# Kernel tuning notes

Measured on AMD Instinct MI355X. Metric: run time of the kernel, lower is better.

Reference implementation:

```python
import jax, jax.numpy as jnp
import numpy as np

B, C, FRAMES, E, W = 8, 2, 3999, 512, 16
STEP = W // 2  # frame_step = W//2 = 8


def setup_inputs() -> dict:
    key = jax.random.key(0)
    k1, k2 = jax.random.split(key)
    dec_input = jax.random.normal(k1, (B, C, FRAMES, E), dtype=jnp.float32)
    weight = jax.random.normal(k2, (W, E), dtype=jnp.float32) * (1.0 / np.sqrt(E))
    return {"dec_input": dec_input, "weight": weight}


def overlap_and_add(signal, frame_step):
    # signal: [..., frames, frame_length] -> [..., (frames-1)*step + frame_length]
    frames, frame_length = signal.shape[-2], signal.shape[-1]
    output_size = frame_step * (frames - 1) + frame_length
    # target sample index of every element of `signal`
    idx = (jnp.arange(frames)[:, None] * frame_step
           + jnp.arange(frame_length)[None, :]).reshape(-1)  # [frames*frame_length]
    flat = signal.reshape(*signal.shape[:-2], frames * frame_length)
    out = jnp.zeros((*signal.shape[:-2], output_size), dtype=signal.dtype)
    # scatter-accumulate overlapping frames along the last axis
    return out.at[..., idx].add(flat)


def reference(dec_input, weight):
    # dec_input: [B, C, frames, E]; weight: [W, E] (nn.Linear(E, W, bias=False))
    est_source = jnp.einsum('bcle,we->bclw', dec_input, weight)  # [B, C, frames, W]
    return overlap_and_add(est_source, STEP)  # [B, C, T]
```

## Files before the change

kernel.cpp:

```cpp
#include <hip/hip_runtime.h>
#include <cstdint>
#include <cstddef>


#define NBC     16
#define FRAMES  3999
#define EE      512
#define TOUT    32000
#define NGROUP  4000
#define GPB     63
#define KCH     64
#define NKCH    8
#define XSTR    65


__global__ __launch_bounds__(256) void decoder_kernel(
    const float* __restrict__ dec,
    const float* __restrict__ wgt,
    float* __restrict__ out)
{
    __shared__ float wl[16 * EE];
    __shared__ float xs[64 * XSTR];

    const int tid   = threadIdx.x;
    const int bc    = blockIdx.x >> 6;
    const int chunk = blockIdx.x & 63;
    const int g0    = chunk * GPB;

    const float* decb = dec + (size_t)bc * (FRAMES * EE);

    {
        const float4* ws = (const float4*)wgt;
        float4*       wd = (float4*)wl;
        #pragma unroll
        for (int i = 0; i < 8; ++i)
            wd[tid + 256 * i] = ws[tid + 256 * i];
    }

    const int s = tid & 63;
    const int q = tid >> 6;
    const int f = g0 - 1 + s;
    const float vmask = (f >= 0 && f < FRAMES) ? 1.0f : 0.0f;

    const int rs = tid >> 4;
    const int c4 = tid & 15;

    float acc[16];
    #pragma unroll
    for (int w = 0; w < 16; ++w) acc[w] = 0.f;

    for (int kk = 0; kk < NKCH; ++kk) {
        __syncthreads();

        #pragma unroll
        for (int it = 0; it < 4; ++it) {
            const int r = rs + 16 * it;
            int fr = g0 - 1 + r;
            fr = min(max(fr, 0), FRAMES - 1);
            const float4 v =
                *(const float4*)(decb + (size_t)fr * EE + kk * KCH + 4 * c4);
            float* x = &xs[r * XSTR + 4 * c4];
            x[0] = v.x; x[1] = v.y; x[2] = v.z; x[3] = v.w;
        }
        __syncthreads();

        float xv[16];
        #pragma unroll
        for (int u = 0; u < 16; ++u)
            xv[u] = xs[s * XSTR + 16 * q + u];
        #pragma unroll
        for (int w = 0; w < 16; ++w) {
            const float4* wrow =
                (const float4*)&wl[w * EE + kk * KCH + 16 * q];
            float sum = 0.f;
            #pragma unroll
            for (int u = 0; u < 4; ++u) {
                const float4 wq = wrow[u];
                sum += xv[4*u+0]*wq.x + xv[4*u+1]*wq.y
                     + xv[4*u+2]*wq.z + xv[4*u+3]*wq.w;
            }
            acc[w] += sum;
        }
    }

    __syncthreads();
    float* red = xs;
    #pragma unroll
    for (int w = 0; w < 16; ++w)
        red[(q * 16 + w) * 64 + s] = acc[w] * vmask;
    __syncthreads();

    for (int o = tid; o < GPB * 8; o += 256) {
        const int j = o >> 3;
        const int i = o & 7;
        const int g = g0 + j;
        if (g < NGROUP) {
            float v = 0.f;
            #pragma unroll
            for (int qq = 0; qq < 4; ++qq)
                v += red[(qq * 16 + i) * 64 + (j + 1)]
                   + red[(qq * 16 + 8 + i) * 64 + j];
            out[(size_t)bc * TOUT + g * 8 + i] = v;
        }
    }
}

extern "C" void kernel_launch(void* const* d_in, const int* in_sizes, int n_in,
                              void* d_out, int out_size, void* d_ws, size_t ws_size,
                              hipStream_t stream) {
    const float* dec = (const float*)d_in[0];
    const float* wgt = (const float*)d_in[1];
    float* out = (float*)d_out;

    decoder_kernel<<<dim3(1024), dim3(256), 0, stream>>>(dec, wgt, out);
}
```

Baseline: 221.2 us.

## Load decoder rows directly into registers, dropping shared-memory staging of inputs

```diff
diff --git a/kernel.cpp b/kernel.cpp
--- a/kernel.cpp
+++ b/kernel.cpp
@@ -9,25 +9,20 @@
 #define TOUT    32000
 #define NGROUP  4000
 #define GPB     63
-#define KCH     64
-#define NKCH    8
-#define XSTR    65
 
-
-__global__ __launch_bounds__(256) void decoder_kernel(
+__global__ __launch_bounds__(256, 4) void decoder_kernel(
     const float* __restrict__ dec,
     const float* __restrict__ wgt,
     float* __restrict__ out)
 {
-    __shared__ float wl[16 * EE];
-    __shared__ float xs[64 * XSTR];
+    __shared__ float smem[16 * EE];
+    float* wl  = smem;
+    float* red = smem;
 
     const int tid   = threadIdx.x;
     const int bc    = blockIdx.x >> 6;
     const int chunk = blockIdx.x & 63;
     const int g0    = chunk * GPB;
-
-    const float* decb = dec + (size_t)bc * (FRAMES * EE);
 
     {
         const float4* ws = (const float4*)wgt;
@@ -36,55 +31,43 @@
         for (int i = 0; i < 8; ++i)
             wd[tid + 256 * i] = ws[tid + 256 * i];
     }
+    __syncthreads();
 
     const int s = tid & 63;
     const int q = tid >> 6;
     const int f = g0 - 1 + s;
     const float vmask = (f >= 0 && f < FRAMES) ? 1.0f : 0.0f;
+    const int fr = min(max(f, 0), FRAMES - 1);
 
-    const int rs = tid >> 4;
-    const int c4 = tid & 15;
+    const float* arow = dec + ((size_t)bc * FRAMES + fr) * EE + q * 128;
+    const float* wbase = wl + q * 128;
 
     float acc[16];
     #pragma unroll
     for (int w = 0; w < 16; ++w) acc[w] = 0.f;
 
-    for (int kk = 0; kk < NKCH; ++kk) {
-        __syncthreads();
+    #pragma unroll
+    for (int c = 0; c < 8; ++c) {
+        float4 xv[4];
+        #pragma unroll
+        for (int u = 0; u < 4; ++u)
+            xv[u] = *(const float4*)(arow + c * 16 + 4 * u);
 
         #pragma unroll
-        for (int it = 0; it < 4; ++it) {
-            const int r = rs + 16 * it;
-            int fr = g0 - 1 + r;
-            fr = min(max(fr, 0), FRAMES - 1);
-            const float4 v =
-                *(const float4*)(decb + (size_t)fr * EE + kk * KCH + 4 * c4);
-            float* x = &xs[r * XSTR + 4 * c4];
-            x[0] = v.x; x[1] = v.y; x[2] = v.z; x[3] = v.w;
-        }
-        __syncthreads();
-
-        float xv[16];
-        #pragma unroll
-        for (int u = 0; u < 16; ++u)
-            xv[u] = xs[s * XSTR + 16 * q + u];
-        #pragma unroll
         for (int w = 0; w < 16; ++w) {
-            const float4* wrow =
-                (const float4*)&wl[w * EE + kk * KCH + 16 * q];
+            const float4* wrow = (const float4*)(wbase + w * EE + c * 16);
             float sum = 0.f;
             #pragma unroll
             for (int u = 0; u < 4; ++u) {
                 const float4 wq = wrow[u];
-                sum += xv[4*u+0]*wq.x + xv[4*u+1]*wq.y
-                     + xv[4*u+2]*wq.z + xv[4*u+3]*wq.w;
+                sum += xv[u].x * wq.x + xv[u].y * wq.y
+                     + xv[u].z * wq.z + xv[u].w * wq.w;
             }
             acc[w] += sum;
         }
     }
 
     __syncthreads();
-    float* red = xs;
     #pragma unroll
     for (int w = 0; w < 16; ++w)
         red[(q * 16 + w) * 64 + s] = acc[w] * vmask;
```

New measurement: 196.8 us. -11.1%, faster.
